# Optimization experiments

Hardware: AMD Instinct MI355X
Metric: run time of the kernel (lower is better)

Reference implementation:

```python
import jax, jax.numpy as jnp
import numpy as np

D_MODEL = 1024
NUM_HEADS = 16
HEAD_DIM = D_MODEL // NUM_HEADS
B, T = 4, 2048


def setup_inputs() -> dict:
    key = jax.random.key(0)
    ks = jax.random.split(key, 11)
    s = 0.02
    return {
        "q": jax.random.normal(ks[0], (B, T, D_MODEL), jnp.float32),
        "k": jax.random.normal(ks[1], (B, T, D_MODEL), jnp.float32),
        "v": jax.random.normal(ks[2], (B, T, D_MODEL), jnp.float32),
        "Wq": jax.random.normal(ks[3], (D_MODEL, D_MODEL), jnp.float32) * s,
        "bq": jnp.zeros((D_MODEL,), jnp.float32),
        "Wk": jax.random.normal(ks[4], (D_MODEL, D_MODEL), jnp.float32) * s,
        "bk": jnp.zeros((D_MODEL,), jnp.float32),
        "Wv": jax.random.normal(ks[5], (D_MODEL, D_MODEL), jnp.float32) * s,
        "bv": jnp.zeros((D_MODEL,), jnp.float32),
        "Wo": jax.random.normal(ks[6], (D_MODEL, D_MODEL), jnp.float32) * s,
        "bo": jnp.zeros((D_MODEL,), jnp.float32),
    }


def reference(q, k, v, Wq, bq, Wk, bk, Wv, bv, Wo, bo):
    Bq, Tq, _ = q.shape
    Tk = k.shape[1]
    # Linear projections then split heads: [B, H, T, Dh]
    qh = (q @ Wq + bq).reshape(Bq, Tq, NUM_HEADS, HEAD_DIM).transpose(0, 2, 1, 3)
    kh = (k @ Wk + bk).reshape(Bq, Tk, NUM_HEADS, HEAD_DIM).transpose(0, 2, 1, 3)
    vh = (v @ Wv + bv).reshape(Bq, Tk, NUM_HEADS, HEAD_DIM).transpose(0, 2, 1, 3)
    scale = 1.0 / jnp.sqrt(jnp.asarray(HEAD_DIM, qh.dtype))
    scores = jnp.einsum("bhqd,bhkd->bhqk", qh, kh) * scale  # [B,H,Tq,Tk]
    attn = jax.nn.softmax(scores, axis=-1)
    # dropout p=0.0 (eval) -> identity
    out = jnp.einsum("bhqk,bhkd->bhqd", attn, vh)  # [B,H,Tq,Dh]
    out = out.transpose(0, 2, 1, 3).reshape(Bq, Tq, D_MODEL)
    return out @ Wo + bo
```

## Files before the change

### kernel.cpp

```cpp
#include <hip/hip_runtime.h>
#include <cstdint>

#define DEV static __device__ __forceinline__

typedef unsigned short u16;
typedef unsigned int u32;
typedef __attribute__((ext_vector_type(8))) _Float16 half8;
typedef __attribute__((ext_vector_type(4))) float f32x4;
typedef __attribute__((ext_vector_type(4))) unsigned short u16x4;

DEV u16 f2h_bits(float f) {
  _Float16 h = (_Float16)f;
  union { _Float16 h; u16 u; } cv; cv.h = h; return cv.u;
}

DEV u32 pack2h(float a, float b) {
  union { __fp16 __attribute__((ext_vector_type(2))) h; u32 u; } cv;
  cv.h = __builtin_amdgcn_cvt_pkrtz(a, b);
  return cv.u;
}

DEV void async_cp16(const void* g, void* l) {
  __builtin_amdgcn_global_load_lds(
      (const __attribute__((address_space(1))) void*)g,
      (__attribute__((address_space(3))) void*)l, 16, 0, 0);
}

__global__ void cvt_f16(const float4* __restrict__ in, u16* __restrict__ out) {
  const int i = blockIdx.x * 256 + threadIdx.x;
  float4 f = in[i];
  u16x4 u;
  u.x = f2h_bits(f.x); u.y = f2h_bits(f.y); u.z = f2h_bits(f.z); u.w = f2h_bits(f.w);
  *(u16x4*)(out + i * 4) = u;
}

struct TParams { const float* W[4]; u16* out[4]; };

__global__ void tcvt4(TParams p) {
  __shared__ float tile[32][33];
  const int w = blockIdx.x >> 10;
  const int bidx = blockIdx.x & 1023;
  const float* __restrict__ Wf = p.W[w];
  u16* __restrict__ Wt = p.out[w];
  const int bx = bidx & 31, by = bidx >> 5;
  const int tx = threadIdx.x & 31, ty = threadIdx.x >> 5;
#pragma unroll
  for (int r = 0; r < 32; r += 8)
    tile[ty + r][tx] = Wf[(by * 32 + ty + r) * 1024 + bx * 32 + tx];
  __syncthreads();
#pragma unroll
  for (int r = 0; r < 32; r += 8)
    Wt[(bx * 32 + ty + r) * 1024 + by * 32 + tx] = f2h_bits(tile[tx][ty + r]);
}

template<int EPI, typename OutT>
DEV void gemm_body(const u16* __restrict__ A, const u16* __restrict__ Bt,
                   const float* __restrict__ bias, OutT* __restrict__ out,
                   u16 (*As)[8192], u16 (*Bs)[8192])
{
  const int tid = threadIdx.x;
  const int wave = tid >> 6, lane = tid & 63;
  const int l15 = lane & 15, lg = lane >> 4;
  const int bid = ((blockIdx.x & 7) << 6) | (blockIdx.x >> 3);
  const int bm = bid >> 3, bn = bid & 7;
  const int m0 = bm * 128, n0 = bn * 128;
  const int wr = wave >> 1, wc = wave & 1;

  const f32x4 fz = {0.f, 0.f, 0.f, 0.f};
  f32x4 acc[4][4];
#pragma unroll
  for (int m = 0; m < 4; ++m)
#pragma unroll
    for (int n = 0; n < 4; ++n) acc[m][n] = fz;

  const char* srcA[4]; const char* srcB[4]; int dstAB[4];
#pragma unroll
  for (int j = 0; j < 4; ++j) {
    const int x = (j * 256 + tid) * 16;
    const int row = x >> 7, colb = x & 127;
    const int pc = colb ^ ((row & 7) << 4);
    srcA[j] = (const char*)A  + (size_t)(m0 + row) * 2048 + pc;
    srcB[j] = (const char*)Bt + (size_t)(n0 + row) * 2048 + pc;
    dstAB[j] = x;
  }

#define STAGE_G(buf, T)                                                     \
  do {                                                                      \
    _Pragma("unroll") for (int j = 0; j < 4; ++j)                           \
      async_cp16(srcA[j] + (size_t)(T) * 128, (char*)As[buf] + dstAB[j]);   \
    _Pragma("unroll") for (int j = 0; j < 4; ++j)                           \
      async_cp16(srcB[j] + (size_t)(T) * 128, (char*)Bs[buf] + dstAB[j]);   \
  } while (0)

  STAGE_G(0, 0);
  asm volatile("s_waitcnt vmcnt(0)" ::: "memory");
  __builtin_amdgcn_s_barrier();
  __builtin_amdgcn_sched_barrier(0);

#define GEMM_IT(T, BR, BS)                                                  \
  do {                                                                      \
    if ((T) < 15) STAGE_G(BS, (T) + 1);                                     \
    half8 af[2][4], bf[2][4];                                               \
    _Pragma("unroll") for (int kk = 0; kk < 2; ++kk)                        \
      _Pragma("unroll") for (int m = 0; m < 4; ++m) {                       \
        const int row = wr * 64 + m * 16 + l15;                             \
        af[kk][m] = *(const half8*)((const char*)As[BR] +                   \
            ((row * 128 + kk * 64 + lg * 16) ^ ((row & 7) << 4)));          \
      }                                                                     \
    _Pragma("unroll") for (int kk = 0; kk < 2; ++kk)                        \
      _Pragma("unroll") for (int n = 0; n < 4; ++n) {                       \
        const int row = wc * 64 + n * 16 + l15;                             \
        bf[kk][n] = *(const half8*)((const char*)Bs[BR] +                   \
            ((row * 128 + kk * 64 + lg * 16) ^ ((row & 7) << 4)));          \
      }                                                                     \
    _Pragma("unroll") for (int kk = 0; kk < 2; ++kk)                        \
      _Pragma("unroll") for (int m = 0; m < 4; ++m)                         \
        _Pragma("unroll") for (int n = 0; n < 4; ++n)                       \
          acc[m][n] = __builtin_amdgcn_mfma_f32_16x16x32_f16(af[kk][m], bf[kk][n], acc[m][n], 0, 0, 0); \
    if ((T) < 15) {                                                         \
      asm volatile("s_waitcnt vmcnt(0)" ::: "memory");                      \
      __builtin_amdgcn_s_barrier();                                         \
      __builtin_amdgcn_sched_barrier(0);                                    \
    }                                                                       \
  } while (0)

  for (int tb = 0; tb < 16; tb += 2) {
    GEMM_IT(tb,     0, 1);
    GEMM_IT(tb + 1, 1, 0);
  }
#undef GEMM_IT
#undef STAGE_G

#pragma unroll
  for (int m = 0; m < 4; ++m) {
    const int Rb = m0 + wr * 64 + m * 16 + lg * 4;
#pragma unroll
    for (int n = 0; n < 4; ++n) {
      const int C = n0 + wc * 64 + n * 16 + l15;
      const float bv = bias[C];
#pragma unroll
      for (int i = 0; i < 4; ++i) {
        const int R = Rb + i;
        const float vv = acc[m][n][i] + bv;
        if (EPI == 3) {
          ((float*)out)[(size_t)R * 1024 + C] = vv;
        } else {
          const int b = R >> 11, t = R & 2047, hh = C >> 6, d = C & 63;
          if (EPI == 0)
            ((u16*)out)[((b * 16 + hh) * 2048 + t) * 64 + d] = f2h_bits(vv * 0.18033688f);
          else if (EPI == 1)
            ((u16*)out)[((b * 16 + hh) * 2048 + t) * 64 + d] = f2h_bits(vv);
          else
            ((u16*)out)[((b * 16 + hh) * 64 + d) * 2048 + t] = f2h_bits(vv);
        }
      }
    }
  }
}

template<int EPI>
__launch_bounds__(256, 2)
__global__ void gemm_proj(const u16* __restrict__ A, const u16* __restrict__ Bt,
                          const float* __restrict__ bias, u16* __restrict__ out)
{
  __shared__ u16 As[2][8192];
  __shared__ u16 Bs[2][8192];
  gemm_body<EPI, u16>(A, Bt, bias, out, As, Bs);
}

__launch_bounds__(256, 2)
__global__ void gemm_o(const u16* __restrict__ A, const u16* __restrict__ Bt,
                       const float* __restrict__ bias, float* __restrict__ out)
{
  __shared__ u16 As[2][8192];
  __shared__ u16 Bs[2][8192];
  gemm_body<3, float>(A, Bt, bias, out, As, Bs);
}

__launch_bounds__(256)
__global__ void attn_kernel(const u16* __restrict__ qh, const u16* __restrict__ kh,
                            const u16* __restrict__ vt, u16* __restrict__ O)
{
  __shared__ u16 Ks[2][4096];
  __shared__ u16 Vs[2][4096];
  const int tid = threadIdx.x, wave = tid >> 6, lane = tid & 63;
  const int l15 = lane & 15, lg = lane >> 4;
  const int swz = ((blockIdx.x & 7) << 7) | (blockIdx.x >> 3);
  const int bh = swz >> 4;
  const int q0 = (swz & 15) << 7;
  const int b = bh >> 4, h = bh & 15;

  const char* qbase = (const char*)(qh + (size_t)(bh * 2048 + q0) * 64);
  const char* kbase = (const char*)(kh + (size_t)bh * 2048 * 64);
  const char* vbase = (const char*)(vt + (size_t)bh * 64 * 2048);

  const bool isK = wave < 2;
  const char* ksrc[4]; int kdst[4];
  const char* vsrc[4]; int vdstA[4], vdstB[4];
#pragma unroll
  for (int j = 0; j < 4; ++j) {
    if (isK) {
      const int x = (wave * 4 + j) * 1024 + lane * 16;
      const int row = x >> 7;
      ksrc[j] = kbase + (x ^ ((row & 7) << 4));
      kdst[j] = x;
      vsrc[j] = nullptr; vdstA[j] = vdstB[j] = 0;
    } else {
      const int u = (wave - 2) * 256 + j * 64 + lane;
      const int d = u >> 3, a = u & 7;
      vsrc[j] = vbase + (size_t)d * 4096 + a * 16;
      const int n = a >> 1;
      const int s1 = 32 * (n >> 1) + 16 * (a & 1) + 4 * (n & 1);
      const int sw = (d & 7) << 4;
      vdstA[j] = (d * 128 + 2 * s1) ^ sw;
      vdstB[j] = (d * 128 + 2 * s1 + 16) ^ sw;
      ksrc[j] = nullptr; kdst[j] = 0;
    }
  }

#pragma unroll
  for (int j = 0; j < 4; ++j) {
    const int x = (j * 256 + tid) * 16;
    const int row = x >> 7;
    async_cp16(qbase + (x ^ ((row & 7) << 4)), (char*)Ks + x);
  }
  __syncthreads();
  half8 aq[2][2];
#pragma unroll
  for (int G = 0; G < 2; ++G) {
    const int qr = wave * 32 + G * 16 + l15;
#pragma unroll
    for (int hh = 0; hh < 2; ++hh) {
      const int addr = (qr * 128 + hh * 64 + lg * 16) ^ ((qr & 7) << 4);
      aq[G][hh] = *(const half8*)((const char*)Ks + addr);
    }
  }
  asm volatile("s_waitcnt lgkmcnt(0)" ::: "memory");
  __syncthreads();

  uint4 va[4];
  if (isK) {
#pragma unroll
    for (int j = 0; j < 4; ++j) async_cp16(ksrc[j], (char*)Ks[0] + kdst[j]);
    asm volatile("s_waitcnt vmcnt(0)" ::: "memory");
  } else {
#pragma unroll
    for (int j = 0; j < 4; ++j) {
      uint4 v = *(const uint4*)(vsrc[j]);
      uint2 w0; w0.x = v.x; w0.y = v.y;
      uint2 w1; w1.x = v.z; w1.y = v.w;
      *(uint2*)((char*)Vs[0] + vdstA[j]) = w0;
      *(uint2*)((char*)Vs[0] + vdstB[j]) = w1;
    }
#pragma unroll
    for (int j = 0; j < 4; ++j) va[j] = *(const uint4*)(vsrc[j] + 128);
    asm volatile("s_waitcnt lgkmcnt(0)" ::: "memory");
  }
  __builtin_amdgcn_s_barrier();
  __builtin_amdgcn_sched_barrier(0);

  half8 ones;
#pragma unroll
  for (int i = 0; i < 8; ++i) ones[i] = (_Float16)1.0f;

  const f32x4 fz = {0.f, 0.f, 0.f, 0.f};
  f32x4 o[4][2], osum[2];
#pragma unroll
  for (int i = 0; i < 4; ++i) { o[i][0] = fz; o[i][1] = fz; }
  osum[0] = fz; osum[1] = fz;

#define ATTN_IT(T, BR, BS)                                                      \
  do {                                                                          \
    const int t_ = (T);                                                         \
    if (isK) {                                                                  \
      if (t_ < 31) {                                                            \
        _Pragma("unroll") for (int j = 0; j < 4; ++j)                           \
          async_cp16(ksrc[j] + (size_t)(t_ + 1) * 8192, (char*)Ks[BS] + kdst[j]); \
      }                                                                         \
    } else {                                                                    \
      if (t_ < 31) {                                                            \
        _Pragma("unroll") for (int j = 0; j < 4; ++j) {                         \
          uint2 w0; w0.x = va[j].x; w0.y = va[j].y;                             \
          uint2 w1; w1.x = va[j].z; w1.y = va[j].w;                             \
          *(uint2*)((char*)Vs[BS] + vdstA[j]) = w0;                             \
          *(uint2*)((char*)Vs[BS] + vdstB[j]) = w1;                             \
        }                                                                       \
        if (t_ < 30) {                                                          \
          _Pragma("unroll") for (int j = 0; j < 4; ++j)                         \
            va[j] = *(const uint4*)(vsrc[j] + (size_t)(t_ + 2) * 128);          \
        }                                                                       \
      }                                                                         \
    }                                                                           \
    f32x4 s[4][2];                                                              \
    __builtin_amdgcn_s_setprio(1);                                              \
    _Pragma("unroll") for (int n = 0; n < 4; ++n) {                             \
      const int krow = n * 16 + l15;                                            \
      const int a0 = (krow * 128 + lg * 16) ^ ((krow & 7) << 4);                \
      half8 bk0 = *(const half8*)((const char*)Ks[BR] + a0);                    \
      half8 bk1 = *(const half8*)((const char*)Ks[BR] + (a0 ^ 64));             \
      s[n][0] = __builtin_amdgcn_mfma_f32_16x16x32_f16(bk0, aq[0][0], fz, 0, 0, 0); \
      s[n][0] = __builtin_amdgcn_mfma_f32_16x16x32_f16(bk1, aq[0][1], s[n][0], 0, 0, 0); \
      s[n][1] = __builtin_amdgcn_mfma_f32_16x16x32_f16(bk0, aq[1][0], fz, 0, 0, 0); \
      s[n][1] = __builtin_amdgcn_mfma_f32_16x16x32_f16(bk1, aq[1][1], s[n][1], 0, 0, 0); \
    }                                                                           \
    __builtin_amdgcn_s_setprio(0);                                              \
    half8 pa[2][2];                                                             \
    _Pragma("unroll") for (int G = 0; G < 2; ++G)                               \
      _Pragma("unroll") for (int hh = 0; hh < 2; ++hh) {                        \
        union { u32 w[4]; half8 hv; } cv;                                       \
        cv.w[0] = pack2h(exp2f(s[2*hh][G][0]),   exp2f(s[2*hh][G][1]));         \
        cv.w[1] = pack2h(exp2f(s[2*hh][G][2]),   exp2f(s[2*hh][G][3]));         \
        cv.w[2] = pack2h(exp2f(s[2*hh+1][G][0]), exp2f(s[2*hh+1][G][1]));       \
        cv.w[3] = pack2h(exp2f(s[2*hh+1][G][2]), exp2f(s[2*hh+1][G][3]));       \
        pa[G][hh] = cv.hv;                                                      \
      }                                                                         \
    __builtin_amdgcn_s_setprio(1);                                              \
    _Pragma("unroll") for (int G = 0; G < 2; ++G) {                             \
      osum[G] = __builtin_amdgcn_mfma_f32_16x16x32_f16(pa[G][0], ones, osum[G], 0, 0, 0); \
      osum[G] = __builtin_amdgcn_mfma_f32_16x16x32_f16(pa[G][1], ones, osum[G], 0, 0, 0); \
    }                                                                           \
    _Pragma("unroll") for (int nd = 0; nd < 4; ++nd) {                          \
      const int dr = nd * 16 + l15;                                             \
      const int a0 = (dr * 128 + lg * 16) ^ ((dr & 7) << 4);                    \
      half8 bv0 = *(const half8*)((const char*)Vs[BR] + a0);                    \
      half8 bv1 = *(const half8*)((const char*)Vs[BR] + (a0 ^ 64));             \
      o[nd][0] = __builtin_amdgcn_mfma_f32_16x16x32_f16(pa[0][0], bv0, o[nd][0], 0, 0, 0); \
      o[nd][0] = __builtin_amdgcn_mfma_f32_16x16x32_f16(pa[0][1], bv1, o[nd][0], 0, 0, 0); \
      o[nd][1] = __builtin_amdgcn_mfma_f32_16x16x32_f16(pa[1][0], bv0, o[nd][1], 0, 0, 0); \
      o[nd][1] = __builtin_amdgcn_mfma_f32_16x16x32_f16(pa[1][1], bv1, o[nd][1], 0, 0, 0); \
    }                                                                           \
    __builtin_amdgcn_s_setprio(0);                                              \
    if (t_ < 31) {                                                              \
      if (isK) asm volatile("s_waitcnt vmcnt(0)" ::: "memory");                 \
      else     asm volatile("s_waitcnt lgkmcnt(0)" ::: "memory");               \
      __builtin_amdgcn_s_barrier();                                             \
      __builtin_amdgcn_sched_barrier(0);                                        \
    }                                                                           \
  } while (0)

  for (int tb = 0; tb < 32; tb += 2) {
    ATTN_IT(tb,     0, 1);
    ATTN_IT(tb + 1, 1, 0);
  }
#undef ATTN_IT

#pragma unroll
  for (int G = 0; G < 2; ++G)
#pragma unroll
    for (int i = 0; i < 4; ++i) {
      const float inv = 1.f / osum[G][i];
      const int t = q0 + wave * 32 + G * 16 + lg * 4 + i;
      u16* orow = O + ((size_t)(b * 2048 + t)) * 1024 + h * 64;
#pragma unroll
      for (int nd = 0; nd < 4; ++nd)
        orow[nd * 16 + l15] = f2h_bits(o[nd][G][i] * inv);
    }
}

extern "C" void kernel_launch(void* const* d_in, const int* in_sizes, int n_in,
                              void* d_out, int out_size, void* d_ws, size_t ws_size,
                              hipStream_t stream)
{
  const float* q  = (const float*)d_in[0];
  const float* k  = (const float*)d_in[1];
  const float* v  = (const float*)d_in[2];
  const float* Wq = (const float*)d_in[3];
  const float* bq = (const float*)d_in[4];
  const float* Wk = (const float*)d_in[5];
  const float* bk = (const float*)d_in[6];
  const float* Wv = (const float*)d_in[7];
  const float* bv = (const float*)d_in[8];
  const float* Wo = (const float*)d_in[9];
  const float* bo = (const float*)d_in[10];

  u16* W = (u16*)d_ws;
  const unsigned MB = 1u << 20;
  u16* wtq = W + 0 * MB;
  u16* wtk = W + 1 * MB;
  u16* wtv = W + 2 * MB;
  u16* wto = W + 3 * MB;
  u16* qhb = W + 4 * MB;
  u16* khb = W + 12 * MB;
  u16* vtb = W + 20 * MB;
  u16* Xb  = W + 28 * MB;

  TParams tp;
  tp.W[0] = Wq; tp.W[1] = Wk; tp.W[2] = Wv; tp.W[3] = Wo;
  tp.out[0] = wtq; tp.out[1] = wtk; tp.out[2] = wtv; tp.out[3] = wto;
  tcvt4<<<4096, 256, 0, stream>>>(tp);

  cvt_f16<<<8192, 256, 0, stream>>>((const float4*)q, Xb);
  gemm_proj<0><<<512, 256, 0, stream>>>(Xb, wtq, bq, qhb);
  cvt_f16<<<8192, 256, 0, stream>>>((const float4*)k, Xb);
  gemm_proj<1><<<512, 256, 0, stream>>>(Xb, wtk, bk, khb);
  cvt_f16<<<8192, 256, 0, stream>>>((const float4*)v, Xb);
  gemm_proj<2><<<512, 256, 0, stream>>>(Xb, wtv, bv, vtb);

  attn_kernel<<<1024, 256, 0, stream>>>(qhb, khb, vtb, Xb);

  gemm_o<<<512, 256, 0, stream>>>(Xb, wto, bo, (float*)d_out);
}
```

Measured before the change: 240.0 us.

## Double attention block to 256 query rows with 8 waves sharing K/V tiles

The attention kernel now launches 512 blocks of 512 threads, each covering 256 query rows instead of 128. Each K/V tile staged in shared memory is therefore reused by twice as many waves, which halves global K/V traffic and per-row staging work. Loader work per wave halves: four waves load K and four load V. The trade-off is fewer, larger blocks, heavier barriers across 8 waves, and possibly lower occupancy. The epilogue is not shown, so it is unclear whether it was updated for the new wave count.

```diff
diff --git a/kernel.cpp b/kernel.cpp
--- a/kernel.cpp
+++ b/kernel.cpp
@@ -177,36 +177,38 @@
   gemm_body<3, float>(A, Bt, bias, out, As, Bs);
 }
 
-__launch_bounds__(256)
+__launch_bounds__(512)
 __global__ void attn_kernel(const u16* __restrict__ qh, const u16* __restrict__ kh,
                             const u16* __restrict__ vt, u16* __restrict__ O)
 {
-  __shared__ u16 Ks[2][4096];
-  __shared__ u16 Vs[2][4096];
+  __shared__ u16 SM[16384];
   const int tid = threadIdx.x, wave = tid >> 6, lane = tid & 63;
   const int l15 = lane & 15, lg = lane >> 4;
-  const int swz = ((blockIdx.x & 7) << 7) | (blockIdx.x >> 3);
-  const int bh = swz >> 4;
-  const int q0 = (swz & 15) << 7;
+  const int swz = ((blockIdx.x & 7) << 6) | (blockIdx.x >> 3);
+  const int bh = swz >> 3;
+  const int q0 = (swz & 7) << 8;
   const int b = bh >> 4, h = bh & 15;
 
   const char* qbase = (const char*)(qh + (size_t)(bh * 2048 + q0) * 64);
   const char* kbase = (const char*)(kh + (size_t)bh * 2048 * 64);
   const char* vbase = (const char*)(vt + (size_t)bh * 64 * 2048);
 
-  const bool isK = wave < 2;
-  const char* ksrc[4]; int kdst[4];
-  const char* vsrc[4]; int vdstA[4], vdstB[4];
-#pragma unroll
-  for (int j = 0; j < 4; ++j) {
+  char* Kbuf[2] = { (char*)SM,         (char*)SM + 8192 };
+  char* Vbuf[2] = { (char*)SM + 16384, (char*)SM + 24576 };
+
+  const bool isK = wave < 4;
+  const char* ksrc[2]; int kdst[2];
+  const char* vsrc[2]; int vdstA[2], vdstB[2];
+#pragma unroll
+  for (int j = 0; j < 2; ++j) {
     if (isK) {
-      const int x = (wave * 4 + j) * 1024 + lane * 16;
-      const int row = x >> 7;
-      ksrc[j] = kbase + (x ^ ((row & 7) << 4));
-      kdst[j] = x;
+      const int yb = wave * 2048 + j * 1024 + lane * 16;
+      const int row = yb >> 7;
+      ksrc[j] = kbase + (yb ^ ((row & 7) << 4));
+      kdst[j] = yb;
       vsrc[j] = nullptr; vdstA[j] = vdstB[j] = 0;
     } else {
-      const int u = (wave - 2) * 256 + j * 64 + lane;
+      const int u = (wave - 4) * 128 + j * 64 + lane;
       const int d = u >> 3, a = u & 7;
       vsrc[j] = vbase + (size_t)d * 4096 + a * 16;
       const int n = a >> 1;
@@ -220,9 +222,9 @@
 
 #pragma unroll
   for (int j = 0; j < 4; ++j) {
-    const int x = (j * 256 + tid) * 16;
+    const int x = j * 8192 + tid * 16;
     const int row = x >> 7;
-    async_cp16(qbase + (x ^ ((row & 7) << 4)), (char*)Ks + x);
+    async_cp16(qbase + (x ^ ((row & 7) << 4)), (char*)SM + x);
   }
   __syncthreads();
   half8 aq[2][2];
@@ -232,28 +234,28 @@
 #pragma unroll
     for (int hh = 0; hh < 2; ++hh) {
       const int addr = (qr * 128 + hh * 64 + lg * 16) ^ ((qr & 7) << 4);
-      aq[G][hh] = *(const half8*)((const char*)Ks + addr);
+      aq[G][hh] = *(const half8*)((const char*)SM + addr);
     }
   }
   asm volatile("s_waitcnt lgkmcnt(0)" ::: "memory");
   __syncthreads();
 
-  uint4 va[4];
+  uint4 va[2];
   if (isK) {
-#pragma unroll
-    for (int j = 0; j < 4; ++j) async_cp16(ksrc[j], (char*)Ks[0] + kdst[j]);
+    async_cp16(ksrc[0], Kbuf[0] + kdst[0]);
+    async_cp16(ksrc[1], Kbuf[0] + kdst[1]);
     asm volatile("s_waitcnt vmcnt(0)" ::: "memory");
   } else {
 #pragma unroll
-    for (int j = 0; j < 4; ++j) {
+    for (int j = 0; j < 2; ++j) {
       uint4 v = *(const uint4*)(vsrc[j]);
       uint2 w0; w0.x = v.x; w0.y = v.y;
       uint2 w1; w1.x = v.z; w1.y = v.w;
-      *(uint2*)((char*)Vs[0] + vdstA[j]) = w0;
-      *(uint2*)((char*)Vs[0] + vdstB[j]) = w1;
+      *(uint2*)(Vbuf[0] + vdstA[j]) = w0;
+      *(uint2*)(Vbuf[0] + vdstB[j]) = w1;
     }
 #pragma unroll
-    for (int j = 0; j < 4; ++j) va[j] = *(const uint4*)(vsrc[j] + 128);
+    for (int j = 0; j < 2; ++j) va[j] = *(const uint4*)(vsrc[j] + 128);
     asm volatile("s_waitcnt lgkmcnt(0)" ::: "memory");
   }
   __builtin_amdgcn_s_barrier();
@@ -274,19 +276,19 @@
     const int t_ = (T);                                                         \
     if (isK) {                                                                  \
       if (t_ < 31) {                                                            \
-        _Pragma("unroll") for (int j = 0; j < 4; ++j)                           \
-          async_cp16(ksrc[j] + (size_t)(t_ + 1) * 8192, (char*)Ks[BS] + kdst[j]); \
+        async_cp16(ksrc[0] + (size_t)(t_ + 1) * 8192, Kbuf[BS] + kdst[0]);      \
+        async_cp16(ksrc[1] + (size_t)(t_ + 1) * 8192, Kbuf[BS] + kdst[1]);      \
       }                                                                         \
     } else {                                                                    \
       if (t_ < 31) {                                                            \
-        _Pragma("unroll") for (int j = 0; j < 4; ++j) {                         \
+        _Pragma("unroll") for (int j = 0; j < 2; ++j) {                         \
           uint2 w0; w0.x = va[j].x; w0.y = va[j].y;                             \
           uint2 w1; w1.x = va[j].z; w1.y = va[j].w;                             \
-          *(uint2*)((char*)Vs[BS] + vdstA[j]) = w0;                             \
-          *(uint2*)((char*)Vs[BS] + vdstB[j]) = w1;                             \
+          *(uint2*)(Vbuf[BS] + vdstA[j]) = w0;                                  \
+          *(uint2*)(Vbuf[BS] + vdstB[j]) = w1;                                  \
         }                                                                       \
         if (t_ < 30) {                                                          \
-          _Pragma("unroll") for (int j = 0; j < 4; ++j)                         \
+          _Pragma("unroll") for (int j = 0; j < 2; ++j)                         \
             va[j] = *(const uint4*)(vsrc[j] + (size_t)(t_ + 2) * 128);          \
         }                                                                       \
       }                                                                         \
@@ -296,8 +298,8 @@
     _Pragma("unroll") for (int n = 0; n < 4; ++n) {                             \
       const int krow = n * 16 + l15;                                            \
       const int a0 = (krow * 128 + lg * 16) ^ ((krow & 7) << 4);                \
-      half8 bk0 = *(const half8*)((const char*)Ks[BR] + a0);                    \
-      half8 bk1 = *(const half8*)((const char*)Ks[BR] + (a0 ^ 64));             \
+      half8 bk0 = *(const half8*)(Kbuf[BR] + a0);                               \
+      half8 bk1 = *(const half8*)(Kbuf[BR] + (a0 ^ 64));                        \
       s[n][0] = __builtin_amdgcn_mfma_f32_16x16x32_f16(bk0, aq[0][0], fz, 0, 0, 0); \
       s[n][0] = __builtin_amdgcn_mfma_f32_16x16x32_f16(bk1, aq[0][1], s[n][0], 0, 0, 0); \
       s[n][1] = __builtin_amdgcn_mfma_f32_16x16x32_f16(bk0, aq[1][0], fz, 0, 0, 0); \
@@ -322,8 +324,8 @@
     _Pragma("unroll") for (int nd = 0; nd < 4; ++nd) {                          \
       const int dr = nd * 16 + l15;                                             \
       const int a0 = (dr * 128 + lg * 16) ^ ((dr & 7) << 4);                    \
-      half8 bv0 = *(const half8*)((const char*)Vs[BR] + a0);                    \
-      half8 bv1 = *(const half8*)((const char*)Vs[BR] + (a0 ^ 64));             \
+      half8 bv0 = *(const half8*)(Vbuf[BR] + a0);                               \
+      half8 bv1 = *(const half8*)(Vbuf[BR] + (a0 ^ 64));                        \
       o[nd][0] = __builtin_amdgcn_mfma_f32_16x16x32_f16(pa[0][0], bv0, o[nd][0], 0, 0, 0); \
       o[nd][0] = __builtin_amdgcn_mfma_f32_16x16x32_f16(pa[0][1], bv1, o[nd][0], 0, 0, 0); \
       o[nd][1] = __builtin_amdgcn_mfma_f32_16x16x32_f16(pa[1][0], bv0, o[nd][1], 0, 0, 0); \
@@ -396,7 +398,7 @@
   cvt_f16<<<8192, 256, 0, stream>>>((const float4*)v, Xb);
   gemm_proj<2><<<512, 256, 0, stream>>>(Xb, wtv, bv, vtb);
 
-  attn_kernel<<<1024, 256, 0, stream>>>(qhb, khb, vtb, Xb);
+  attn_kernel<<<512, 512, 0, stream>>>(qhb, khb, vtb, Xb);
 
   gemm_o<<<512, 256, 0, stream>>>(Xb, wto, bo, (float*)d_out);
 }
```

After: 237.4 us. About the same (-1.1%).
